# Kernel tuning notes

Hardware: AMD Instinct MI355X
Metric: run time of the kernel (lower is better)

The kernel has to match this reference:

```python
import jax, jax.numpy as jnp
import numpy as np

N, E = 50000, 800000
IN_C, HID, OUT_C = 128, 64, 40

def setup_inputs() -> dict:
    key = jax.random.key(0)
    ks = jax.random.split(key, 16)
    def w(k, shape, fan_in):
        return jax.random.normal(k, shape, dtype=jnp.float32) * (1.0 / np.sqrt(fan_in))
    x = jax.random.normal(ks[0], (N, IN_C), dtype=jnp.float32)
    edge_index = jax.random.randint(ks[1], (2, E), 0, N, dtype=jnp.int64)
    return {
        "x": x,
        "edge_index": edge_index,
        "W1": w(ks[2], (IN_C, HID), IN_C), "b1": jnp.zeros((HID,), jnp.float32),
        "W2": w(ks[3], (HID, HID), HID),   "b2": jnp.zeros((HID,), jnp.float32),
        "W3": w(ks[4], (HID, HID), HID),   "b3": jnp.zeros((HID,), jnp.float32),
        "g1": jnp.ones((HID,), jnp.float32), "be1": jnp.zeros((HID,), jnp.float32),
        "g2": jnp.ones((HID,), jnp.float32), "be2": jnp.zeros((HID,), jnp.float32),
        "M1": w(ks[5], (HID, HID), HID),   "mb1": jnp.zeros((HID,), jnp.float32),
        "M2": w(ks[6], (HID, OUT_C), HID), "mb2": jnp.zeros((OUT_C,), jnp.float32),
        "batch_size": N,
    }

def reference(x, edge_index, W1, b1, W2, b2, W3, b3, g1, be1, g2, be2, M1, mb1, M2, mb2, batch_size):
    src, dst = edge_index[0], edge_index[1]
    n = x.shape[0]
    # GCN symmetric norm with self-loops: deg over destination, +1 for self loop
    deg = jax.ops.segment_sum(jnp.ones(src.shape[0], x.dtype), dst, num_segments=n) + 1.0
    dinv = jax.lax.rsqrt(deg)  # deg >= 1 always
    enorm = (dinv[src] * dinv[dst])[:, None]  # [E,1]
    sloop = (dinv * dinv)[:, None]            # [N,1] self-loop norm

    def gcn_conv(h, W, b):
        hw = h @ W                                              # [N,H] transform first
        agg = jax.ops.segment_sum(enorm * hw[src], dst, num_segments=n)
        return agg + sloop * hw + b

    def layer_norm(h, g, be):
        mu = jnp.mean(h, axis=-1, keepdims=True)
        var = jnp.var(h, axis=-1, keepdims=True)
        return (h - mu) * jax.lax.rsqrt(var + 1e-5) * g + be

    h = jax.nn.relu(layer_norm(gcn_conv(x, W1, b1), g1, be1))
    h = jax.nn.relu(layer_norm(gcn_conv(h, W2, b2), g2, be2))
    h = gcn_conv(h, W3, b3)
    # MLP: Linear -> ReLU -> Linear
    h = jax.nn.relu(h @ M1 + mb1) @ M2 + mb2
    return jax.nn.softmax(h[:batch_size], axis=1)
```

## Files before the change

kernel.cpp:

```cpp
#include <hip/hip_runtime.h>
#include <hip/hip_fp16.h>
#include <math.h>

#define HID   64
#define OUTC  40
#define CAP   64

__global__ void zero_kernel(int4* __restrict__ p, int n4) {
    int i = blockIdx.x * blockDim.x + threadIdx.x;
    if (i < n4) p[i] = make_int4(0, 0, 0, 0);
}

__global__ void fill_kernel(const int* __restrict__ src, const int* __restrict__ dst,
                            int* __restrict__ cnt, unsigned short* __restrict__ recs,
                            int E, int N) {
    int g    = blockIdx.x & 7;
    int gblk = blockIdx.x >> 3;
    int nblk = gridDim.x >> 3;
    int slice = (N + 7) >> 3;
    int lo = g * slice;
    int hi = lo + slice; if (hi > N) hi = N;
    for (int e = gblk * blockDim.x + threadIdx.x; e < E; e += nblk * blockDim.x) {
        int d = dst[e];
        if (d >= lo && d < hi) {
            int pos = atomicAdd(&cnt[d], 1);
            if (pos < CAP) recs[(size_t)d * CAP + pos] = (unsigned short)src[e];
        }
    }
}

#define FMA16(acc, a, b) \
    acc[0][0] = fmaf(a.x, b.x, acc[0][0]); acc[0][1] = fmaf(a.x, b.y, acc[0][1]); \
    acc[0][2] = fmaf(a.x, b.z, acc[0][2]); acc[0][3] = fmaf(a.x, b.w, acc[0][3]); \
    acc[1][0] = fmaf(a.y, b.x, acc[1][0]); acc[1][1] = fmaf(a.y, b.y, acc[1][1]); \
    acc[1][2] = fmaf(a.y, b.z, acc[1][2]); acc[1][3] = fmaf(a.y, b.w, acc[1][3]); \
    acc[2][0] = fmaf(a.z, b.x, acc[2][0]); acc[2][1] = fmaf(a.z, b.y, acc[2][1]); \
    acc[2][2] = fmaf(a.z, b.z, acc[2][2]); acc[2][3] = fmaf(a.z, b.w, acc[2][3]); \
    acc[3][0] = fmaf(a.w, b.x, acc[3][0]); acc[3][1] = fmaf(a.w, b.y, acc[3][1]); \
    acc[3][2] = fmaf(a.w, b.z, acc[3][2]); acc[3][3] = fmaf(a.w, b.w, acc[3][3]);

template<int CIN, typename T>
__global__ __launch_bounds__(256) void xform_kernel(const T* __restrict__ X,
                                                    const float* __restrict__ W,
                                                    const int* __restrict__ cnt,
                                                    __half* __restrict__ out, int N) {
    __shared__ float Xs[CIN][68];
    __shared__ float Ws[CIN][68];
    int tid = threadIdx.x;
    int base = blockIdx.x << 6;
    int rows = N - base; if (rows > 64) rows = 64;

    {
        int k = tid >> 4, c = (tid & 15) << 2;
        #pragma unroll
        for (int k0 = 0; k0 < CIN; k0 += 16) {
            float4 wv = *(const float4*)(W + (size_t)((k0 + k) << 6) + c);
            *(float4*)&Ws[k0 + k][c] = wv;
        }
    }
    {
        int r = tid >> 2, q = (tid & 3) << 2;
        int rc = r < rows ? r : 0;
        const T* xp = X + (size_t)(base + rc) * CIN + q;
        #pragma unroll
        for (int k0 = 0; k0 < CIN; k0 += 16) {
            float4 xv;
            if constexpr (sizeof(T) == 4) {
                xv = *(const float4*)(xp + k0);
            } else {
                union { uint2 u; __half2 h[2]; } pk;
                pk.u = *(const uint2*)(xp + k0);
                float2 f01 = __half22float2(pk.h[0]);
                float2 f23 = __half22float2(pk.h[1]);
                xv = make_float4(f01.x, f01.y, f23.x, f23.y);
            }
            Xs[k0 + q + 0][r] = xv.x;
            Xs[k0 + q + 1][r] = xv.y;
            Xs[k0 + q + 2][r] = xv.z;
            Xs[k0 + q + 3][r] = xv.w;
        }
    }
    __syncthreads();

    int tx = tid & 15, ty = tid >> 4;
    float acc[4][4] = {};
    #pragma unroll 4
    for (int k = 0; k < CIN; k++) {
        float4 a = *(const float4*)&Xs[k][ty << 2];
        float4 b = *(const float4*)&Ws[k][tx << 2];
        FMA16(acc, a, b)
    }
    #pragma unroll
    for (int rr = 0; rr < 4; rr++) {
        int row = (ty << 2) + rr;
        if (row < rows) {
            float di = rsqrtf((float)cnt[base + row] + 1.0f);
            union { uint2 u; __half2 h[2]; } pk;
            pk.h[0] = __float22half2_rn(make_float2(acc[rr][0] * di, acc[rr][1] * di));
            pk.h[1] = __float22half2_rn(make_float2(acc[rr][2] * di, acc[rr][3] * di));
            *(uint2*)(out + ((size_t)(base + row) << 6) + (tx << 2)) = pk.u;
        }
    }
    if (blockIdx.x == gridDim.x - 1 && tid < 8) {
        uint4 z = make_uint4(0, 0, 0, 0);
        ((uint4*)(out + ((size_t)N << 6)))[tid] = z;
    }
}

template<bool LN>
__global__ void conv_kernel(const __half* __restrict__ hwh,
                            const unsigned short* __restrict__ recs,
                            const int* __restrict__ cnt,
                            const float* __restrict__ b, const float* __restrict__ g,
                            const float* __restrict__ be, __half* __restrict__ out, int N) {
    int lane = threadIdx.x & 63;
    int row  = (blockIdx.x << 2) + (threadIdx.x >> 6);
    if (row >= N) return;

    int cn = cnt[row];
    int c  = cn > CAP ? CAP : cn;
    int s_l = N;
    if (lane < c) s_l = recs[(size_t)row * CAP + lane];

    int g8 = lane >> 3, j = lane & 7;
    const uint4* hw16 = (const uint4*)hwh;
    float di = rsqrtf((float)cn + 1.0f);
    uint4 selfv = hw16[(size_t)row * 8 + j];

    float acc[8] = {0,0,0,0,0,0,0,0};
    int kmax = (c + 15) & ~15;
    for (int k = 0; k < kmax; k += 16) {
        int s0 = __shfl(s_l, k + g8), s1 = __shfl(s_l, k + 8 + g8);
        uint4 v0 = hw16[(size_t)s0 * 8 + j];
        uint4 v1 = hw16[(size_t)s1 * 8 + j];
        const __half2* h0 = (const __half2*)&v0;
        const __half2* h1 = (const __half2*)&v1;
        #pragma unroll
        for (int t = 0; t < 4; t++) {
            float2 f0 = __half22float2(h0[t]);
            float2 f1 = __half22float2(h1[t]);
            acc[2*t]   += f0.x + f1.x;
            acc[2*t+1] += f0.y + f1.y;
        }
    }
    #pragma unroll
    for (int off = 8; off < 64; off <<= 1) {
        #pragma unroll
        for (int t = 0; t < 8; t++) acc[t] += __shfl_xor(acc[t], off);
    }

    int f0 = j << 3;
    const __half2* sp = (const __half2*)&selfv;
    float bb[8];
    *(float4*)&bb[0] = *(const float4*)(b + f0);
    *(float4*)&bb[4] = *(const float4*)(b + f0 + 4);
    #pragma unroll
    for (int t = 0; t < 4; t++) {
        float2 f = __half22float2(sp[t]);
        acc[2*t]   = fmaf(di, acc[2*t]   + f.x, bb[2*t]);
        acc[2*t+1] = fmaf(di, acc[2*t+1] + f.y, bb[2*t+1]);
    }

    if (LN) {
        float s = 0.f;
        #pragma unroll
        for (int t = 0; t < 8; t++) s += acc[t];
        #pragma unroll
        for (int o = 1; o < 8; o <<= 1) s += __shfl_xor(s, o);
        float mu = s * (1.f / 64.f);
        float v = 0.f;
        #pragma unroll
        for (int t = 0; t < 8; t++) { acc[t] -= mu; v += acc[t] * acc[t]; }
        #pragma unroll
        for (int o = 1; o < 8; o <<= 1) v += __shfl_xor(v, o);
        float r = rsqrtf(v * (1.f / 64.f) + 1e-5f);
        float gg[8], eb[8];
        *(float4*)&gg[0] = *(const float4*)(g + f0);
        *(float4*)&gg[4] = *(const float4*)(g + f0 + 4);
        *(float4*)&eb[0] = *(const float4*)(be + f0);
        *(float4*)&eb[4] = *(const float4*)(be + f0 + 4);
        #pragma unroll
        for (int t = 0; t < 8; t++)
            acc[t] = fmaxf(fmaf(acc[t] * r, gg[t], eb[t]), 0.f);
    }
    if (g8 == 0) {
        union { uint4 u; __half2 h[4]; } pk;
        #pragma unroll
        for (int t = 0; t < 4; t++)
            pk.h[t] = __float22half2_rn(make_float2(acc[2*t], acc[2*t+1]));
        *(uint4*)(out + (size_t)row * 64 + f0) = pk.u;
    }
}

__global__ __launch_bounds__(256) void mlp_kernel(const __half* __restrict__ h,
                           const float* __restrict__ M1, const float* __restrict__ mb1,
                           const float* __restrict__ M2, const float* __restrict__ mb2,
                           float* __restrict__ out, int N) {
    __shared__ float Hs [64][68];
    __shared__ float W1s[64][68];
    __shared__ float H2s[64][68];
    __shared__ float W2s[64][44];
    int tid = threadIdx.x;
    int base = blockIdx.x << 6;
    int rows = N - base; if (rows > 64) rows = 64;

    {
        int k = tid >> 4, c = (tid & 15) << 2;
        #pragma unroll
        for (int k0 = 0; k0 < 64; k0 += 16) {
            float4 wv = *(const float4*)(M1 + (size_t)((k0 + k) << 6) + c);
            *(float4*)&W1s[k0 + k][c] = wv;
        }
    }
    for (int i = tid; i < 64 * OUTC; i += 256)
        W2s[i / OUTC][i % OUTC] = M2[i];
    {
        int r = tid >> 2, q = (tid & 3) << 2;
        int rc = r < rows ? r : 0;
        const __half* xp = h + (((size_t)(base + rc)) << 6) + q;
        #pragma unroll
        for (int k0 = 0; k0 < 64; k0 += 16) {
            union { uint2 u; __half2 hh[2]; } pk;
            pk.u = *(const uint2*)(xp + k0);
            float2 f01 = __half22float2(pk.hh[0]);
            float2 f23 = __half22float2(pk.hh[1]);
            Hs[k0 + q + 0][r] = f01.x;
            Hs[k0 + q + 1][r] = f01.y;
            Hs[k0 + q + 2][r] = f23.x;
            Hs[k0 + q + 3][r] = f23.y;
        }
    }
    __syncthreads();

    int tx = tid & 15, ty = tid >> 4;

    float acc[4][4] = {};
    #pragma unroll 4
    for (int k = 0; k < 64; k++) {
        float4 a = *(const float4*)&Hs[k][ty << 2];
        float4 b = *(const float4*)&W1s[k][tx << 2];
        FMA16(acc, a, b)
    }
    float4 b1v = *(const float4*)(mb1 + (tx << 2));
    #pragma unroll
    for (int cc = 0; cc < 4; cc++) {
        float bc = cc == 0 ? b1v.x : cc == 1 ? b1v.y : cc == 2 ? b1v.z : b1v.w;
        #pragma unroll
        for (int rr = 0; rr < 4; rr++)
            H2s[(tx << 2) + cc][(ty << 2) + rr] = fmaxf(acc[rr][cc] + bc, 0.f);
    }
    __syncthreads();

    int bx = (tx < 10) ? (tx << 2) : 0;
    float acc2[4][4] = {};
    #pragma unroll 4
    for (int k = 0; k < 64; k++) {
        float4 a = *(const float4*)&H2s[k][ty << 2];
        float4 b = *(const float4*)&W2s[k][bx];
        FMA16(acc2, a, b)
    }
    float4 b2v = *(const float4*)(mb2 + bx);

    #pragma unroll
    for (int rr = 0; rr < 4; rr++) {
        float v0 = acc2[rr][0] + b2v.x, v1 = acc2[rr][1] + b2v.y;
        float v2 = acc2[rr][2] + b2v.z, v3 = acc2[rr][3] + b2v.w;
        float m = fmaxf(fmaxf(v0, v1), fmaxf(v2, v3));
        if (tx >= 10) m = -1e30f;
        #pragma unroll
        for (int s = 1; s < 16; s <<= 1) m = fmaxf(m, __shfl_xor(m, s));
        float e0 = __expf(v0 - m), e1 = __expf(v1 - m);
        float e2 = __expf(v2 - m), e3 = __expf(v3 - m);
        float sum = (tx < 10) ? (e0 + e1) + (e2 + e3) : 0.f;
        #pragma unroll
        for (int s = 1; s < 16; s <<= 1) sum += __shfl_xor(sum, s);
        float inv = 1.f / sum;
        int row = (ty << 2) + rr;
        if (tx < 10 && row < rows)
            *(float4*)(out + (size_t)(base + row) * OUTC + bx) =
                make_float4(e0 * inv, e1 * inv, e2 * inv, e3 * inv);
    }
}

extern "C" void kernel_launch(void* const* d_in, const int* in_sizes, int n_in,
                              void* d_out, int out_size, void* d_ws, size_t ws_size,
                              hipStream_t stream) {
    const float* x   = (const float*)d_in[0];
    const int*   ei  = (const int*)  d_in[1];
    const float* W1  = (const float*)d_in[2];
    const float* b1  = (const float*)d_in[3];
    const float* W2  = (const float*)d_in[4];
    const float* b2  = (const float*)d_in[5];
    const float* W3  = (const float*)d_in[6];
    const float* b3  = (const float*)d_in[7];
    const float* g1  = (const float*)d_in[8];
    const float* be1 = (const float*)d_in[9];
    const float* g2  = (const float*)d_in[10];
    const float* be2 = (const float*)d_in[11];
    const float* M1  = (const float*)d_in[12];
    const float* mb1 = (const float*)d_in[13];
    const float* M2  = (const float*)d_in[14];
    const float* mb2 = (const float*)d_in[15];

    const int IN_C = 128;
    int N = in_sizes[0] / IN_C;
    int E = in_sizes[1] / 2;
    const int* src = ei;
    const int* dst = ei + E;

    char* ws = (char*)d_ws;
    size_t off = 0;
    auto carve = [&](size_t bytes) -> void* {
        void* p = ws + off;
        off = (off + bytes + 255) & ~(size_t)255;
        return p;
    };
    int*            cnt  = (int*)           carve(((size_t)N + 4) * sizeof(int));
    unsigned short* recs = (unsigned short*)carve((size_t)N * CAP * sizeof(unsigned short));
    __half*         HWh  = (__half*)        carve((size_t)(N + 1) * HID * sizeof(__half));
    __half*         H    = (__half*)        carve((size_t)(N + 1) * HID * sizeof(__half));
    __half*         PH   = (__half*)        carve((size_t)(N + 1) * HID * sizeof(__half));

    int n4 = (N + 3) / 4;
    zero_kernel<<<(n4 + 255) / 256, 256, 0, stream>>>((int4*)cnt, n4);

    int rb = (N + 3) / 4;
    int tb = (N + 63) / 64;

    fill_kernel<<<2048, 256, 0, stream>>>(src, dst, cnt, recs, E, N);

    xform_kernel<128, float><<<tb, 256, 0, stream>>>(x, W1, cnt, HWh, N);
    conv_kernel<true><<<rb, 256, 0, stream>>>(HWh, recs, cnt, b1, g1, be1, H, N);
    xform_kernel<64, __half><<<tb, 256, 0, stream>>>(H, W2, cnt, HWh, N);
    conv_kernel<true><<<rb, 256, 0, stream>>>(HWh, recs, cnt, b2, g2, be2, H, N);
    xform_kernel<64, __half><<<tb, 256, 0, stream>>>(H, W3, cnt, HWh, N);
    conv_kernel<false><<<rb, 256, 0, stream>>>(HWh, recs, cnt, b3, nullptr, nullptr, PH, N);

    mlp_kernel<<<tb, 256, 0, stream>>>(PH, M1, mb1, M2, mb2, (float*)d_out, N);
}
```

Baseline: 186.8 us.

## Fuse final GCN aggregation with MLP and softmax into one kernel

Replaces the last conv_kernel and mlp_kernel with a single 1024-thread kernel. Each block first gathers and aggregates neighbor features for its 64 rows directly into shared memory, then runs the two small matmuls and the softmax. This removes the fp16 PH intermediate round trip through global memory and one launch, and keeps the layer-3 output in fp32 rather than rounding it to half. The per-thread GEMM work shrinks to one output row and four columns, and each wave now aggregates four rows in sequence, which may lower gather parallelism per block.

```diff
diff --git a/kernel.cpp b/kernel.cpp
--- a/kernel.cpp
+++ b/kernel.cpp
@@ -192,13 +192,15 @@
     }
 }
 
-__global__ __launch_bounds__(256) void mlp_kernel(const __half* __restrict__ h,
-                           const float* __restrict__ M1, const float* __restrict__ mb1,
-                           const float* __restrict__ M2, const float* __restrict__ mb2,
-                           float* __restrict__ out, int N) {
-    __shared__ float Hs [64][68];
+__global__ __launch_bounds__(1024) void convmlp_kernel(
+        const __half* __restrict__ hwh, const unsigned short* __restrict__ recs,
+        const int* __restrict__ cnt, const float* __restrict__ b3,
+        const float* __restrict__ M1, const float* __restrict__ mb1,
+        const float* __restrict__ M2, const float* __restrict__ mb2,
+        float* __restrict__ out, int N) {
+    __shared__ float Hs [64][65];
+    __shared__ float H2s[64][65];
     __shared__ float W1s[64][68];
-    __shared__ float H2s[64][68];
     __shared__ float W2s[64][44];
     int tid = threadIdx.x;
     int base = blockIdx.x << 6;
@@ -206,80 +208,115 @@
 
     {
         int k = tid >> 4, c = (tid & 15) << 2;
-        #pragma unroll
-        for (int k0 = 0; k0 < 64; k0 += 16) {
-            float4 wv = *(const float4*)(M1 + (size_t)((k0 + k) << 6) + c);
-            *(float4*)&W1s[k0 + k][c] = wv;
-        }
-    }
-    for (int i = tid; i < 64 * OUTC; i += 256)
+        *(float4*)&W1s[k][c] = *(const float4*)(M1 + ((size_t)k << 6) + c);
+    }
+    for (int i = tid; i < 64 * OUTC; i += 1024)
         W2s[i / OUTC][i % OUTC] = M2[i];
+
+    int lane = tid & 63, w = tid >> 6;
+    int g8 = lane >> 3, j = lane & 7, f0 = j << 3;
+    const uint4* hw16 = (const uint4*)hwh;
+    float bb[8];
+    *(float4*)&bb[0] = *(const float4*)(b3 + f0);
+    *(float4*)&bb[4] = *(const float4*)(b3 + f0 + 4);
+
+    #pragma unroll
+    for (int r = 0; r < 4; r++) {
+        int idx = (r << 4) + w;
+        int row = base + idx;
+        if (row >= N) {
+            if (g8 == 0) {
+                #pragma unroll
+                for (int t = 0; t < 8; t++) Hs[f0 + t][idx] = 0.f;
+            }
+            continue;
+        }
+        int cn = cnt[row];
+        int c = cn > CAP ? CAP : cn;
+        int s_l = N;
+        if (lane < c) s_l = recs[(size_t)row * CAP + lane];
+        float di = rsqrtf((float)cn + 1.0f);
+        uint4 selfv = hw16[(size_t)row * 8 + j];
+
+        float acc[8] = {0,0,0,0,0,0,0,0};
+        int kmax = (c + 15) & ~15;
+        for (int k = 0; k < kmax; k += 16) {
+            int s0 = __shfl(s_l, k + g8), s1 = __shfl(s_l, k + 8 + g8);
+            uint4 v0 = hw16[(size_t)s0 * 8 + j];
+            uint4 v1 = hw16[(size_t)s1 * 8 + j];
+            const __half2* h0 = (const __half2*)&v0;
+            const __half2* h1 = (const __half2*)&v1;
+            #pragma unroll
+            for (int t = 0; t < 4; t++) {
+                float2 a0 = __half22float2(h0[t]);
+                float2 a1 = __half22float2(h1[t]);
+                acc[2*t]   += a0.x + a1.x;
+                acc[2*t+1] += a0.y + a1.y;
+            }
+        }
+        #pragma unroll
+        for (int off = 8; off < 64; off <<= 1) {
+            #pragma unroll
+            for (int t = 0; t < 8; t++) acc[t] += __shfl_xor(acc[t], off);
+        }
+        const __half2* sp = (const __half2*)&selfv;
+        #pragma unroll
+        for (int t = 0; t < 4; t++) {
+            float2 f = __half22float2(sp[t]);
+            acc[2*t]   = fmaf(di, acc[2*t]   + f.x, bb[2*t]);
+            acc[2*t+1] = fmaf(di, acc[2*t+1] + f.y, bb[2*t+1]);
+        }
+        if (g8 == 0) {
+            #pragma unroll
+            for (int t = 0; t < 8; t++) Hs[f0 + t][idx] = acc[t];
+        }
+    }
+    __syncthreads();
+
+    int tx = tid & 15, ty = tid >> 4;
     {
-        int r = tid >> 2, q = (tid & 3) << 2;
-        int rc = r < rows ? r : 0;
-        const __half* xp = h + (((size_t)(base + rc)) << 6) + q;
-        #pragma unroll
-        for (int k0 = 0; k0 < 64; k0 += 16) {
-            union { uint2 u; __half2 hh[2]; } pk;
-            pk.u = *(const uint2*)(xp + k0);
-            float2 f01 = __half22float2(pk.hh[0]);
-            float2 f23 = __half22float2(pk.hh[1]);
-            Hs[k0 + q + 0][r] = f01.x;
-            Hs[k0 + q + 1][r] = f01.y;
-            Hs[k0 + q + 2][r] = f23.x;
-            Hs[k0 + q + 3][r] = f23.y;
-        }
+        float a0 = 0.f, a1 = 0.f, a2 = 0.f, a3 = 0.f;
+        #pragma unroll 4
+        for (int k = 0; k < 64; k++) {
+            float hv = Hs[k][ty];
+            float4 wv = *(const float4*)&W1s[k][tx << 2];
+            a0 = fmaf(hv, wv.x, a0); a1 = fmaf(hv, wv.y, a1);
+            a2 = fmaf(hv, wv.z, a2); a3 = fmaf(hv, wv.w, a3);
+        }
+        float4 b1v = *(const float4*)(mb1 + (tx << 2));
+        int c0 = tx << 2;
+        H2s[c0 + 0][ty] = fmaxf(a0 + b1v.x, 0.f);
+        H2s[c0 + 1][ty] = fmaxf(a1 + b1v.y, 0.f);
+        H2s[c0 + 2][ty] = fmaxf(a2 + b1v.z, 0.f);
+        H2s[c0 + 3][ty] = fmaxf(a3 + b1v.w, 0.f);
     }
     __syncthreads();
 
-    int tx = tid & 15, ty = tid >> 4;
-
-    float acc[4][4] = {};
+    int bx = (tx < 10) ? (tx << 2) : 0;
+    float o0 = 0.f, o1 = 0.f, o2 = 0.f, o3 = 0.f;
     #pragma unroll 4
     for (int k = 0; k < 64; k++) {
-        float4 a = *(const float4*)&Hs[k][ty << 2];
-        float4 b = *(const float4*)&W1s[k][tx << 2];
-        FMA16(acc, a, b)
-    }
-    float4 b1v = *(const float4*)(mb1 + (tx << 2));
-    #pragma unroll
-    for (int cc = 0; cc < 4; cc++) {
-        float bc = cc == 0 ? b1v.x : cc == 1 ? b1v.y : cc == 2 ? b1v.z : b1v.w;
-        #pragma unroll
-        for (int rr = 0; rr < 4; rr++)
-            H2s[(tx << 2) + cc][(ty << 2) + rr] = fmaxf(acc[rr][cc] + bc, 0.f);
-    }
-    __syncthreads();
-
-    int bx = (tx < 10) ? (tx << 2) : 0;
-    float acc2[4][4] = {};
-    #pragma unroll 4
-    for (int k = 0; k < 64; k++) {
-        float4 a = *(const float4*)&H2s[k][ty << 2];
-        float4 b = *(const float4*)&W2s[k][bx];
-        FMA16(acc2, a, b)
+        float hv = H2s[k][ty];
+        float4 wv = *(const float4*)&W2s[k][bx];
+        o0 = fmaf(hv, wv.x, o0); o1 = fmaf(hv, wv.y, o1);
+        o2 = fmaf(hv, wv.z, o2); o3 = fmaf(hv, wv.w, o3);
     }
     float4 b2v = *(const float4*)(mb2 + bx);
-
-    #pragma unroll
-    for (int rr = 0; rr < 4; rr++) {
-        float v0 = acc2[rr][0] + b2v.x, v1 = acc2[rr][1] + b2v.y;
-        float v2 = acc2[rr][2] + b2v.z, v3 = acc2[rr][3] + b2v.w;
-        float m = fmaxf(fmaxf(v0, v1), fmaxf(v2, v3));
-        if (tx >= 10) m = -1e30f;
-        #pragma unroll
-        for (int s = 1; s < 16; s <<= 1) m = fmaxf(m, __shfl_xor(m, s));
-        float e0 = __expf(v0 - m), e1 = __expf(v1 - m);
-        float e2 = __expf(v2 - m), e3 = __expf(v3 - m);
-        float sum = (tx < 10) ? (e0 + e1) + (e2 + e3) : 0.f;
-        #pragma unroll
-        for (int s = 1; s < 16; s <<= 1) sum += __shfl_xor(sum, s);
-        float inv = 1.f / sum;
-        int row = (ty << 2) + rr;
-        if (tx < 10 && row < rows)
-            *(float4*)(out + (size_t)(base + row) * OUTC + bx) =
-                make_float4(e0 * inv, e1 * inv, e2 * inv, e3 * inv);
-    }
+    o0 += b2v.x; o1 += b2v.y; o2 += b2v.z; o3 += b2v.w;
+
+    float m = fmaxf(fmaxf(o0, o1), fmaxf(o2, o3));
+    if (tx >= 10) m = -1e30f;
+    #pragma unroll
+    for (int s = 1; s < 16; s <<= 1) m = fmaxf(m, __shfl_xor(m, s));
+    float e0 = __expf(o0 - m), e1 = __expf(o1 - m);
+    float e2 = __expf(o2 - m), e3 = __expf(o3 - m);
+    float sum = (tx < 10) ? (e0 + e1) + (e2 + e3) : 0.f;
+    #pragma unroll
+    for (int s = 1; s < 16; s <<= 1) sum += __shfl_xor(sum, s);
+    float inv = 1.f / sum;
+    if (tx < 10 && ty < rows)
+        *(float4*)(out + (size_t)(base + ty) * OUTC + bx) =
+            make_float4(e0 * inv, e1 * inv, e2 * inv, e3 * inv);
 }
 
 extern "C" void kernel_launch(void* const* d_in, const int* in_sizes, int n_in,
@@ -319,7 +356,6 @@
     unsigned short* recs = (unsigned short*)carve((size_t)N * CAP * sizeof(unsigned short));
     __half*         HWh  = (__half*)        carve((size_t)(N + 1) * HID * sizeof(__half));
     __half*         H    = (__half*)        carve((size_t)(N + 1) * HID * sizeof(__half));
-    __half*         PH   = (__half*)        carve((size_t)(N + 1) * HID * sizeof(__half));
 
     int n4 = (N + 3) / 4;
     zero_kernel<<<(n4 + 255) / 256, 256, 0, stream>>>((int4*)cnt, n4);
@@ -334,7 +370,6 @@
     xform_kernel<64, __half><<<tb, 256, 0, stream>>>(H, W2, cnt, HWh, N);
     conv_kernel<true><<<rb, 256, 0, stream>>>(HWh, recs, cnt, b2, g2, be2, H, N);
     xform_kernel<64, __half><<<tb, 256, 0, stream>>>(H, W3, cnt, HWh, N);
-    conv_kernel<false><<<rb, 256, 0, stream>>>(HWh, recs, cnt, b3, nullptr, nullptr, PH, N);
-
-    mlp_kernel<<<tb, 256, 0, stream>>>(PH, M1, mb1, M2, mb2, (float*)d_out, N);
-}
+    convmlp_kernel<<<tb, 1024, 0, stream>>>(HWh, recs, cnt, b3, M1, mb1, M2, mb2,
+                                            (float*)d_out, N);
+}
```

New measurement: 196.3 us. 5.1% more time.
